# Kernel tuning notes

Measured on AMD Instinct MI355X. Metric: run time of the kernel, lower is better.

## Reference

```python
import jax, jax.numpy as jnp
import numpy as np

NUM_HEADS = 8
HEAD_DIM = 96
SCALE = HEAD_DIM ** -0.5
STRIDE_Q = (1, 2, 2)
STRIDE_KV = (1, 8, 8)
PAD = [(1, 1), (1, 1), (1, 1)]  # kernel 3 -> padding = 3//2 = 1


def _gelu_pool(t, w, stride, thw):
    """_pre_attention_pool -> GELU -> depthwise Conv3d -> _post_attention_pool.

    t: [B, H, L, hd] flattened tokens; thw = (T, Hs, Ws) with L = T*Hs*Ws.
    Returns pooled [B, H, L', hd] and new thw.
    """
    B, NH, L, C = t.shape
    T, Hs, Ws = thw
    x = t.reshape(B * NH, T, Hs, Ws, C).transpose(0, 4, 1, 2, 3)  # [B*NH, C, T, Hs, Ws]
    x = jax.nn.gelu(x, approximate=False)  # torch F.gelu default (erf)
    x = jax.lax.conv_general_dilated(
        x, w, window_strides=stride, padding=PAD,
        dimension_numbers=('NCDHW', 'OIDHW', 'NCDHW'),
        feature_group_count=C)  # depthwise: groups = head_dim
    new_thw = (x.shape[2], x.shape[3], x.shape[4])
    Lp = new_thw[0] * new_thw[1] * new_thw[2]
    x = x.reshape(B, NH, C, Lp).transpose(0, 1, 3, 2)  # [B, NH, L', C]
    return x, new_thw


def setup_inputs() -> dict:
    key = jax.random.key(0)
    ks = jax.random.split(key, 8)
    B, T, Hs, Ws, C = 2, 8, 56, 56, 768
    L = T * Hs * Ws
    s = 0.02
    return {
        'x': jax.random.normal(ks[0], (B, L, C), jnp.float32),
        'qkv_w': jax.random.normal(ks[1], (3 * C, C), jnp.float32) * s,
        'qkv_b': jnp.zeros((3 * C,), jnp.float32),
        'proj_w': jax.random.normal(ks[2], (C, C), jnp.float32) * s,
        'proj_b': jnp.zeros((C,), jnp.float32),
        'pool_q_w': jax.random.normal(ks[3], (HEAD_DIM, 1, 3, 3, 3), jnp.float32) * 0.1,
        'pool_k_w': jax.random.normal(ks[4], (HEAD_DIM, 1, 3, 3, 3), jnp.float32) * 0.1,
        'pool_v_w': jax.random.normal(ks[5], (HEAD_DIM, 1, 3, 3, 3), jnp.float32) * 0.1,
        't_size': T, 'h_size': Hs, 'w_size': Ws,
    }


def reference(x, qkv_w, qkv_b, proj_w, proj_b, pool_q_w, pool_k_w, pool_v_w,
              t_size, h_size, w_size):
    B, N, C = x.shape
    # fused qkv projection -> [3, B, heads, N, head_dim]
    qkv = (x @ qkv_w.T + qkv_b).reshape(B, N, 3, NUM_HEADS, C // NUM_HEADS)
    qkv = qkv.transpose(2, 0, 3, 1, 4)
    q, k, v = qkv[0], qkv[1], qkv[2]

    thw = (t_size, h_size, w_size)
    q, q_thw = _gelu_pool(q, pool_q_w, STRIDE_Q, thw)
    k, _ = _gelu_pool(k, pool_k_w, STRIDE_KV, thw)
    v, _ = _gelu_pool(v, pool_v_w, STRIDE_KV, thw)

    attn = jax.nn.softmax((q * SCALE) @ jnp.swapaxes(k, -2, -1), axis=-1)
    Nq = q.shape[2]
    out = (attn @ v + q)  # residual_pool=True (iMViT)
    out = out.transpose(0, 2, 1, 3).reshape(B, Nq, C)
    out = out @ proj_w.T + proj_b
    return out
```

## Files before the change

### kernel.cpp

```cpp
#include <hip/hip_runtime.h>
#include <cstdint>

#define NH 8
#define HD 96
#define CDIM 768
#define BQ 2
#define T0 8
#define H0 56
#define W0 56
#define L0 (T0*H0*W0)
#define HP_Q 28
#define WP_Q 28
#define LQ (T0*HP_Q*WP_Q)
#define HP_K 7
#define WP_K 7
#define LK (T0*HP_K*WP_K)
#define LKP 416
#define SCALE 0.10206207261596577f
#define NYC 20
#define MKV 6400

typedef __bf16 bf16;
typedef bf16 bf16x4 __attribute__((ext_vector_type(4)));
typedef bf16 bf16x8 __attribute__((ext_vector_type(8)));
typedef float f32x4 __attribute__((ext_vector_type(4)));
typedef float f4 __attribute__((ext_vector_type(4)));

#define GPTR(x) ((const __attribute__((address_space(1))) void*)(x))
#define LPTR(x) ((__attribute__((address_space(3))) void*)(x))

__device__ __forceinline__ float fast_gelu(float x) {
    float z = __builtin_fabsf(x) * 0.7071067811865476f;
    float p = 1.f + z*(0.278393f + z*(0.230389f + z*(0.000972f + z*0.078108f)));
    p = p * p;
    p = p * p;
    float e = 1.f - __builtin_amdgcn_rcpf(p);
    float erfv = (x < 0.f) ? -e : e;
    return 0.5f * x * (1.f + erfv);
}

__global__ void cvt4(const f4* __restrict__ in, bf16x4* __restrict__ out, long n4) {
    long i = (long)blockIdx.x * blockDim.x + threadIdx.x;
    long stride = (long)gridDim.x * blockDim.x;
    for (; i < n4; i += stride) {
        f4 v = in[i];
        bf16x4 o;
        o.x = (bf16)v.x; o.y = (bf16)v.y; o.z = (bf16)v.z; o.w = (bf16)v.w;
        out[i] = o;
    }
}

__device__ __forceinline__ int cmap(int i) {
    return ((i + 1) / 3) * 8 + (i + 1) % 3 - 1;
}

template<int MODE>
__global__ __launch_bounds__(256) void gemm_bt(
    const bf16* __restrict__ A, const bf16* __restrict__ B,
    const float* __restrict__ bias, void* __restrict__ Out,
    int M, int N, int K, int NBN, int gelu_cols)
{
    __shared__ bf16 sh[2*16384];
    const int tid = threadIdx.x;
    const int lane = tid & 63;
    const int w = tid >> 6;
    const int wr = w >> 1, wc = w & 1;

    const int nwg = gridDim.x;
    const int q_ = nwg >> 3, r_ = nwg & 7;
    const int xcd = blockIdx.x & 7, off = blockIdx.x >> 3;
    const int swz = (xcd < r_ ? xcd*(q_+1) : r_*(q_+1) + (xcd - r_)*q_) + off;
    const long bn = swz % NBN, bm = swz / NBN;

    f32x4 acc[4][4];
#pragma unroll
    for (int i = 0; i < 4; ++i)
#pragma unroll
        for (int j = 0; j < 4; ++j) acc[i][j] = (f32x4){0.f,0.f,0.f,0.f};

    const int trow = tid >> 3;
    const int tchunk = (tid & 7) ^ (trow & 7);

    long aoff[4];
#pragma unroll
    for (int s = 0; s < 4; ++s) {
        int rA = (int)bm*128 + s*32 + trow;
        if (MODE == 2) {
            int mm = rA < MKV ? rA : 0;
            int b = mm / 3200; int r = mm - b*3200;
            int t = r / 400;  int rr = r - t*400;
            int yi = rr / NYC, xi = rr - yi*NYC;
            int y = cmap(yi), x = cmap(xi);
            aoff[s] = ((long)b*L0 + (t*H0 + y)*W0 + x) * (long)K;
        } else {
            aoff[s] = (long)rA * K;
        }
    }
    const bf16* Bg = B + (bn*128 + trow)*(long)K + tchunk*8;

    const int arow = lane & 15;
    const int g8 = (lane >> 4) * 8;
    const int aswz = (arow & 7) * 8;

    auto stage = [&](int buf, int kt) {
        bf16* ldsA = sh + buf*16384;
        bf16* ldsB = sh + buf*16384 + 8192;
#pragma unroll
        for (int s = 0; s < 4; ++s) {
            __builtin_amdgcn_global_load_lds(GPTR(A + aoff[s] + kt*64 + tchunk*8),
                                             LPTR(ldsA + s*2048 + tid*8), 16, 0, 0);
            __builtin_amdgcn_global_load_lds(GPTR(Bg + (long)kt*64 + (long)s*32*K),
                                             LPTR(ldsB + s*2048 + tid*8), 16, 0, 0);
        }
    };
    auto compute = [&](int buf) {
        const bf16* ldsA = sh + buf*16384;
        const bf16* ldsB = sh + buf*16384 + 8192;
#pragma unroll
        for (int kk = 0; kk < 2; ++kk) {
            bf16x8 af[4], bfr[4];
#pragma unroll
            for (int i = 0; i < 4; ++i)
                af[i] = *(const bf16x8*)&ldsA[(wr*64 + i*16 + arow)*64 + ((kk*32 + g8) ^ aswz)];
#pragma unroll
            for (int j = 0; j < 4; ++j)
                bfr[j] = *(const bf16x8*)&ldsB[(wc*64 + j*16 + arow)*64 + ((kk*32 + g8) ^ aswz)];
            __builtin_amdgcn_s_setprio(1);
#pragma unroll
            for (int i = 0; i < 4; ++i)
#pragma unroll
                for (int j = 0; j < 4; ++j)
                    acc[i][j] = __builtin_amdgcn_mfma_f32_16x16x32_bf16(af[i], bfr[j], acc[i][j], 0, 0, 0);
            __builtin_amdgcn_s_setprio(0);
        }
    };

    const int nkt = K / 64;
    stage(0, 0);
    for (int kt = 0; kt < nkt; ++kt) {
        if (kt + 1 < nkt) {
            stage((kt + 1) & 1, kt + 1);
            asm volatile("s_waitcnt vmcnt(8)" ::: "memory");
        } else {
            asm volatile("s_waitcnt vmcnt(0)" ::: "memory");
        }
        __builtin_amdgcn_s_barrier();
        __builtin_amdgcn_sched_barrier(0);
        compute(kt & 1);
        __builtin_amdgcn_sched_barrier(0);
        __builtin_amdgcn_s_barrier();
    }

    if (MODE == 1) {
#pragma unroll
        for (int j = 0; j < 4; ++j) {
            const int col = (int)bn*128 + wc*64 + j*16 + (lane & 15);
            const float bcol = bias[col];
#pragma unroll
            for (int i = 0; i < 4; ++i) {
                int row0 = (int)bm*128 + wr*64 + i*16 + ((lane>>4)<<2);
#pragma unroll
                for (int r = 0; r < 4; ++r)
                    ((float*)Out)[(size_t)(row0 + r)*N + col] = acc[i][j][r] + bcol;
            }
        }
    } else {
        bf16* tls = sh;
#pragma unroll
        for (int j = 0; j < 4; ++j) {
            const int colb = (int)bn*128 + wc*64 + j*16;
            const int lcol = wc*64 + j*16 + (lane & 15);
            const float bcol = bias[colb + (lane & 15)];
            const bool do_gelu = (MODE == 2) || (colb < gelu_cols);
#pragma unroll
            for (int i = 0; i < 4; ++i) {
                int lrow0 = wr*64 + i*16 + ((lane>>4)<<2);
#pragma unroll
                for (int r = 0; r < 4; ++r) {
                    float vacc = acc[i][j][r] + bcol;
                    if (do_gelu) vacc = fast_gelu(vacc);
                    tls[(lrow0 + r)*136 + lcol] = (bf16)vacc;
                }
            }
        }
        __syncthreads();
#pragma unroll
        for (int it = 0; it < 8; ++it) {
            int idx = it*256 + tid;
            int mloc = idx >> 4;
            int ck = idx & 15;
            bf16x8 v = *(const bf16x8*)&tls[mloc*136 + ck*8];
            int m = (int)bm*128 + mloc;
            int col = (int)bn*128 + ck*8;
            if (MODE == 0) {
                int nh = col / HD;
                int c = col - nh*HD;
                int bflag = m >= L0;
                int l = m - (bflag ? L0 : 0);
                size_t addr = ((size_t)(bflag*8 + nh)*L0 + l)*HD + c;
                *(bf16x8*)&((bf16*)Out)[addr] = v;
            } else {
                if (m < MKV) {
                    int part = col / 768;
                    int cb = col - part*768;
                    int nh = cb / HD;
                    int c = cb - nh*HD;
                    int b = m / 3200; int r = m - b*3200;
                    size_t addr = ((size_t)(part*16 + b*8 + nh)*3200 + r)*HD + c;
                    *(bf16x8*)&((bf16*)Out)[addr] = v;
                }
            }
        }
    }
}

__global__ __launch_bounds__(256) void dwconv_q(
    const bf16* __restrict__ in, const float* __restrict__ w,
    bf16* __restrict__ out, int total)
{
    __shared__ float lw[27*HD];
    for (int i = threadIdx.x; i < 27*HD; i += 256) {
        int c = i / 27, tap = i % 27;
        lw[tap*HD + c] = w[i];
    }
    __syncthreads();
    int idx = blockIdx.x*256 + threadIdx.x;
    if (idx >= total) return;
    int c8 = idx % 12;
    int p = idx / 12;
    int xo = p % WP_Q;
    int yo = (p / WP_Q) % HP_Q;
    int bh = p / (WP_Q*HP_Q);
    const bf16* ip = in + (size_t)bh * L0 * HD + c8*8;

    float acc[T0][8];
#pragma unroll
    for (int t = 0; t < T0; ++t)
#pragma unroll
        for (int j = 0; j < 8; ++j) acc[t][j] = 0.f;

#pragma unroll
    for (int dy = 0; dy < 3; ++dy) {
        int y = yo*2 + dy - 1;
        if ((unsigned)y >= (unsigned)H0) continue;
#pragma unroll
        for (int dx = 0; dx < 3; ++dx) {
            int x = xo*2 + dx - 1;
            if ((unsigned)x >= (unsigned)W0) continue;
            float wreg[3][8];
#pragma unroll
            for (int dt = 0; dt < 3; ++dt)
#pragma unroll
                for (int j = 0; j < 8; ++j)
                    wreg[dt][j] = lw[(dt*9 + dy*3 + dx)*HD + c8*8 + j];
            const bf16* colp = ip + ((size_t)(y*W0 + x))*HD;
#pragma unroll
            for (int t = 0; t < T0; ++t) {
                bf16x8 v = *(const bf16x8*)(colp + (size_t)t*H0*W0*HD);
                float f[8];
#pragma unroll
                for (int j = 0; j < 8; ++j) f[j] = (float)v[j];
#pragma unroll
                for (int dt = 0; dt < 3; ++dt) {
                    int to = t - dt + 1;
                    if (to < 0 || to >= T0) continue;
#pragma unroll
                    for (int j = 0; j < 8; ++j)
                        acc[to][j] += wreg[dt][j] * f[j];
                }
            }
        }
    }

#pragma unroll
    for (int to = 0; to < T0; ++to) {
        int l = (to*HP_Q + yo)*WP_Q + xo;
        bf16x8 ov;
#pragma unroll
        for (int j = 0; j < 8; ++j) ov[j] = (bf16)acc[to][j];
        *(bf16x8*)&out[((size_t)bh*LQ + l)*HD + c8*8] = ov;
    }
}

template<int MODE>
__global__ __launch_bounds__(256) void dwconv_kv(
    const bf16* __restrict__ in, const float* __restrict__ w,
    bf16* __restrict__ out, int total)
{
    __shared__ float lw[27*HD];
    for (int i = threadIdx.x; i < 27*HD; i += 256) {
        int c = i / 27, tap = i % 27;
        lw[tap*HD + c] = w[i];
    }
    __syncthreads();
    int idx = blockIdx.x*256 + threadIdx.x;
    if (idx >= total) return;
    int c8 = idx % 12;
    int p = idx / 12;
    int xo = p % WP_K;
    int yo = (p / WP_K) % HP_K;
    int bh = p / (WP_K*HP_K);
    const bf16* ip = in + (size_t)bh * 3200 * HD + c8*8;

    float acc[T0][8];
#pragma unroll
    for (int t = 0; t < T0; ++t)
#pragma unroll
        for (int j = 0; j < 8; ++j) acc[t][j] = 0.f;

#pragma unroll
    for (int dy = 0; dy < 3; ++dy) {
        int yi = 3*yo + dy - 1;
        if ((unsigned)yi >= (unsigned)NYC) continue;
#pragma unroll
        for (int dx = 0; dx < 3; ++dx) {
            int xi = 3*xo + dx - 1;
            if ((unsigned)xi >= (unsigned)NYC) continue;
            float wreg[3][8];
#pragma unroll
            for (int dt = 0; dt < 3; ++dt)
#pragma unroll
                for (int j = 0; j < 8; ++j)
                    wreg[dt][j] = lw[(dt*9 + dy*3 + dx)*HD + c8*8 + j];
            const bf16* colp = ip + ((size_t)(yi*NYC + xi))*HD;
#pragma unroll
            for (int t = 0; t < T0; ++t) {
                bf16x8 v = *(const bf16x8*)(colp + (size_t)t*400*HD);
                float f[8];
#pragma unroll
                for (int j = 0; j < 8; ++j) f[j] = (float)v[j];
#pragma unroll
                for (int dt = 0; dt < 3; ++dt) {
                    int to = t - dt + 1;
                    if (to < 0 || to >= T0) continue;
#pragma unroll
                    for (int j = 0; j < 8; ++j)
                        acc[to][j] += wreg[dt][j] * f[j];
                }
            }
        }
    }

#pragma unroll
    for (int to = 0; to < T0; ++to) {
        int l = (to*HP_K + yo)*WP_K + xo;
        if (MODE == 2) {
#pragma unroll
            for (int j = 0; j < 8; ++j)
                out[((size_t)bh*HD + c8*8 + j)*LKP + l] = (bf16)acc[to][j];
        } else {
            bf16x8 ov;
#pragma unroll
            for (int j = 0; j < 8; ++j) ov[j] = (bf16)acc[to][j];
            *(bf16x8*)&out[((size_t)bh*LKP + l)*HD + c8*8] = ov;
        }
    }
}

__global__ __launch_bounds__(256) void attn_mfma(
    const bf16* __restrict__ q, const bf16* __restrict__ k,
    const bf16* __restrict__ vt, bf16* __restrict__ out)
{
    const int tid = threadIdx.x;
    const int lane = tid & 63;
    const int w = tid >> 6;
    const int col = lane & 15;
    const int g = lane >> 4;
    const int blk = blockIdx.x;
    const int qblk = blk % (LQ/64);
    const int bh = blk / (LQ/64);
    const int q0 = qblk*64 + w*16;

    const bf16* Qp  = q  + ((size_t)bh*LQ + q0)*HD;
    const bf16* Kp  = k  + (size_t)bh*LKP*HD;
    const bf16* VTp = vt + (size_t)bh*HD*LKP;

    bf16x8 qf[3];
#pragma unroll
    for (int c = 0; c < 3; ++c)
        qf[c] = *(const bf16x8*)&Qp[(size_t)col*HD + c*32 + g*8];

    f32x4 o[6];
#pragma unroll
    for (int t = 0; t < 6; ++t) o[t] = (f32x4){0.f,0.f,0.f,0.f};
    float lsum = 0.f;

    for (int kc = 0; kc < LKP/32; ++kc) {
        const int kvb = kc*32;
        uint32_t P[2][2];
#pragma unroll
        for (int s = 0; s < 2; ++s) {
            f32x4 acc = (f32x4){0.f,0.f,0.f,0.f};
#pragma unroll
            for (int c = 0; c < 3; ++c) {
                bf16x8 kf = *(const bf16x8*)&Kp[(size_t)(kvb + s*16 + col)*HD + c*32 + g*8];
                acc = __builtin_amdgcn_mfma_f32_16x16x32_bf16(kf, qf[c], acc, 0, 0, 0);
            }
            bf16x4 pb;
#pragma unroll
            for (int r = 0; r < 4; ++r) {
                int kv = kvb + s*16 + g*4 + r;
                float p = (kv < LK) ? __expf(acc[r]*SCALE) : 0.f;
                lsum += p;
                pb[r] = (bf16)p;
            }
            union { bf16x4 v; uint32_t u[2]; } pk; pk.v = pb;
            P[s][0] = pk.u[0]; P[s][1] = pk.u[1];
        }
        uint32_t sa0 = (g < 2) ? P[1][0] : P[0][0];
        uint32_t sa1 = (g < 2) ? P[1][1] : P[0][1];
        uint32_t tb0 = (g < 2) ? P[0][0] : P[1][0];
        uint32_t tb1 = (g < 2) ? P[0][1] : P[1][1];
        uint32_t R32_0 = (uint32_t)__shfl_xor((int)sa0, 32);
        uint32_t R32_1 = (uint32_t)__shfl_xor((int)sa1, 32);
        uint32_t R48_0 = (uint32_t)__shfl_xor((int)sa0, 48);
        uint32_t R48_1 = (uint32_t)__shfl_xor((int)sa1, 48);
        uint32_t R16_0 = (uint32_t)__shfl_xor((int)tb0, 16);
        uint32_t R16_1 = (uint32_t)__shfl_xor((int)tb1, 16);
        union { uint32_t u[4]; bf16x8 v; } pf;
        pf.u[0] = (g == 0) ? P[0][0] : (g == 1) ? R48_0 : (g == 2) ? R32_0 : R16_0;
        pf.u[1] = (g == 0) ? P[0][1] : (g == 1) ? R48_1 : (g == 2) ? R32_1 : R16_1;
        pf.u[2] = (g == 0) ? R16_0 : (g == 1) ? R32_0 : (g == 2) ? R48_0 : P[1][0];
        pf.u[3] = (g == 0) ? R16_1 : (g == 1) ? R32_1 : (g == 2) ? R48_1 : P[1][1];
#pragma unroll
        for (int t = 0; t < 6; ++t) {
            bf16x8 vf = *(const bf16x8*)&VTp[(size_t)(t*16 + col)*LKP + kvb + g*8];
            o[t] = __builtin_amdgcn_mfma_f32_16x16x32_bf16(vf, pf.v, o[t], 0, 0, 0);
        }
    }

    lsum += __shfl_xor(lsum, 16);
    lsum += __shfl_xor(lsum, 32);
    float inv = 1.f / lsum;

    const int b = bh >> 3, nh = bh & 7;
    size_t obase = ((size_t)b*LQ + q0 + col)*CDIM + (size_t)nh*HD;
#pragma unroll
    for (int t = 0; t < 6; ++t) {
        bf16x4 qres = *(const bf16x4*)&Qp[(size_t)col*HD + t*16 + g*4];
        bf16x4 ov;
#pragma unroll
        for (int r = 0; r < 4; ++r)
            ov[r] = (bf16)(o[t][r]*inv + (float)qres[r]);
        *(bf16x4*)&out[obase + t*16 + g*4] = ov;
    }
}

extern "C" void kernel_launch(void* const* d_in, const int* in_sizes, int n_in,
                              void* d_out, int out_size, void* d_ws, size_t ws_size,
                              hipStream_t stream) {
    const float* x      = (const float*)d_in[0];
    const float* qkv_w  = (const float*)d_in[1];
    const float* qkv_b  = (const float*)d_in[2];
    const float* proj_w = (const float*)d_in[3];
    const float* proj_b = (const float*)d_in[4];
    const float* pq_w   = (const float*)d_in[5];
    const float* pk_w   = (const float*)d_in[6];
    const float* pv_w   = (const float*)d_in[7];

    uint8_t* ws = (uint8_t*)d_ws;
    bf16* x_bf     = (bf16*)(ws);
    bf16* qg_out   = (bf16*)(ws +  77070336);
    bf16* kv_c     = (bf16*)(ws + 154140672);
    bf16* wqkv_bf  = (bf16*)(ws + 173801472);
    bf16* wproj_bf = (bf16*)(ws + 177340416);
    bf16* q_bf     = (bf16*)(ws + 178520064);
    bf16* k_bf     = (bf16*)(ws + 197787648);
    bf16* vt_bf    = (bf16*)(ws + 199065600);
    bf16* attn_o   = (bf16*)(ws + 200343552);

    hipMemsetAsync(k_bf, 0, 1277952, stream);
    hipMemsetAsync(vt_bf, 0, 1277952, stream);

    cvt4<<<2048, 256, 0, stream>>>((const f4*)x, (bf16x4*)x_bf, 38535168/4);
    cvt4<<<1728, 256, 0, stream>>>((const f4*)qkv_w, (bf16x4*)wqkv_bf, 1769472/4);
    cvt4<<<576, 256, 0, stream>>>((const f4*)proj_w, (bf16x4*)wproj_bf, 589824/4);

    gemm_bt<0><<<392*6, 256, 0, stream>>>(
        x_bf, wqkv_bf, qkv_b, qg_out, 50176, 768, 768, 6, 768);

    gemm_bt<2><<<50*12, 256, 0, stream>>>(
        x_bf, wqkv_bf + (size_t)768*768, qkv_b + 768, kv_c, MKV, 1536, 768, 12, 0);

    dwconv_q<<<588, 256, 0, stream>>>(qg_out, pq_w, q_bf, 16*HP_Q*WP_Q*12);
    dwconv_kv<1><<<37, 256, 0, stream>>>(kv_c, pk_w, k_bf, 16*HP_K*WP_K*12);
    dwconv_kv<2><<<37, 256, 0, stream>>>(kv_c + (size_t)16*3200*HD, pv_w, vt_bf, 16*HP_K*WP_K*12);

    attn_mfma<<<16*(LQ/64), 256, 0, stream>>>(q_bf, k_bf, vt_bf, attn_o);

    gemm_bt<1><<<6*98, 256, 0, stream>>>(
        attn_o, wproj_bf, proj_b, d_out, 12544, 768, 768, 6, 0);
}
```

Baseline: 340.9 us.

## Use 256x256-tile GEMM for Q projection and fuse conversion and KV conv launches

Replaces the 128x128 Q-projection GEMM with a dedicated 512-thread 256x256-tile kernel. It uses direct global-to-LDS loads interleaved with MFMA phases, double buffering, and a GELU epilogue. It also merges the three fp32->bf16 conversions into one launch, and merges the K and V depthwise convs into one launch that zeroes the padding, removing two memsets. The intent is more data reuse in the largest GEMM and less launch overhead, at the cost of higher register/LDS pressure. The MODE 2 row clamp is removed, which may read past MKV rows for the last tile.

```diff
diff --git a/kernel.cpp b/kernel.cpp
--- a/kernel.cpp
+++ b/kernel.cpp
@@ -39,26 +39,164 @@
     return 0.5f * x * (1.f + erfv);
 }
 
-__global__ void cvt4(const f4* __restrict__ in, bf16x4* __restrict__ out, long n4) {
-    long i = (long)blockIdx.x * blockDim.x + threadIdx.x;
+#define NX4 9633792
+#define NW4 442368
+#define NP4 147456
+__global__ void cvt_all(const f4* __restrict__ x, const f4* __restrict__ wq,
+                        const f4* __restrict__ wp, bf16x4* __restrict__ xo,
+                        bf16x4* __restrict__ wqo, bf16x4* __restrict__ wpo) {
+    const long total = (long)NX4 + NW4 + NP4;
     long stride = (long)gridDim.x * blockDim.x;
-    for (; i < n4; i += stride) {
-        f4 v = in[i];
-        bf16x4 o;
-        o.x = (bf16)v.x; o.y = (bf16)v.y; o.z = (bf16)v.z; o.w = (bf16)v.w;
-        out[i] = o;
+    for (long i = (long)blockIdx.x * blockDim.x + threadIdx.x; i < total; i += stride) {
+        f4 v; bf16x4* o;
+        if (i < NX4)            { v = x[i];            o = xo + i; }
+        else if (i < NX4 + NW4) { v = wq[i - NX4];     o = wqo + (i - NX4); }
+        else                    { v = wp[i - NX4 - NW4]; o = wpo + (i - NX4 - NW4); }
+        bf16x4 t;
+        t.x = (bf16)v.x; t.y = (bf16)v.y; t.z = (bf16)v.z; t.w = (bf16)v.w;
+        *o = t;
     }
 }
 
 __device__ __forceinline__ int cmap(int i) {
     return ((i + 1) / 3) * 8 + (i + 1) % 3 - 1;
+}
+
+__global__ __launch_bounds__(512, 2) void gemm256_q(
+    const bf16* __restrict__ A, const bf16* __restrict__ B,
+    const float* __restrict__ bias, bf16* __restrict__ Out)
+{
+    __shared__ bf16 sh[2*32768];
+    const int tid = threadIdx.x;
+    const int lane = tid & 63;
+    const int wid = tid >> 6;
+    const int wm = wid >> 2, wn = wid & 3;
+    const int arow = lane & 15;
+    const int g = lane >> 4;
+    const int srow = tid >> 3;
+    const int schunk = tid & 7;
+    const int csw = schunk ^ (srow & 7);
+    const int K = 768;
+
+    const int nwg = gridDim.x;
+    const int q_ = nwg >> 3, r_ = nwg & 7;
+    const int xcd = blockIdx.x & 7, off = blockIdx.x >> 3;
+    const int swz = (xcd < r_ ? xcd*(q_+1) : r_*(q_+1) + (xcd - r_)*q_) + off;
+    const long bn = swz % 3, bm = swz / 3;
+
+    f32x4 acc[8][4];
+#pragma unroll
+    for (int i = 0; i < 8; ++i)
+#pragma unroll
+        for (int j = 0; j < 4; ++j) acc[i][j] = (f32x4){0.f,0.f,0.f,0.f};
+
+    const bf16* Ab = A + (bm*256 + srow)*(long)K + csw*8;
+    const bf16* Bb = B + (bn*256 + srow)*(long)K + csw*8;
+
+    auto issueA = [&](int buf, int kt, int s) {
+        __builtin_amdgcn_global_load_lds(GPTR(Ab + (long)(s*64)*K + kt*64),
+            LPTR(sh + buf*32768 + s*4096 + tid*8), 16, 0, 0);
+    };
+    auto issueB = [&](int buf, int kt, int s) {
+        __builtin_amdgcn_global_load_lds(GPTR(Bb + (long)(s*64)*K + kt*64),
+            LPTR(sh + buf*32768 + 16384 + s*4096 + tid*8), 16, 0, 0);
+    };
+    auto phase = [&](int buf, int qm, int qn) {
+        const bf16* ldsA = sh + buf*32768;
+        const bf16* ldsB = sh + buf*32768 + 16384;
+        bf16x8 af[4][2], bfr[2][2];
+#pragma unroll
+        for (int i = 0; i < 4; ++i) {
+            int R = wm*128 + (qm*4 + i)*16 + arow;
+#pragma unroll
+            for (int kk = 0; kk < 2; ++kk)
+                af[i][kk] = *(const bf16x8*)&ldsA[R*64 + (((kk*4 + g) ^ (R & 7))*8)];
+        }
+#pragma unroll
+        for (int j = 0; j < 2; ++j) {
+            int R = wn*64 + (qn*2 + j)*16 + arow;
+#pragma unroll
+            for (int kk = 0; kk < 2; ++kk)
+                bfr[j][kk] = *(const bf16x8*)&ldsB[R*64 + (((kk*4 + g) ^ (R & 7))*8)];
+        }
+        asm volatile("s_waitcnt lgkmcnt(0)" ::: "memory");
+        __builtin_amdgcn_sched_barrier(0);
+        __builtin_amdgcn_s_setprio(1);
+#pragma unroll
+        for (int i = 0; i < 4; ++i)
+#pragma unroll
+            for (int j = 0; j < 2; ++j)
+#pragma unroll
+                for (int kk = 0; kk < 2; ++kk)
+                    acc[qm*4 + i][qn*2 + j] = __builtin_amdgcn_mfma_f32_16x16x32_bf16(
+                        af[i][kk], bfr[j][kk], acc[qm*4 + i][qn*2 + j], 0, 0, 0);
+        __builtin_amdgcn_s_setprio(0);
+        __builtin_amdgcn_sched_barrier(0);
+    };
+
+    const int nkt = K / 64;
+#pragma unroll
+    for (int s = 0; s < 4; ++s) { issueA(0, 0, s); issueB(0, 0, s); }
+
+    for (int kt = 0; kt < nkt; ++kt) {
+        const int cur = kt & 1, nxt = cur ^ 1;
+        const bool pre = (kt + 1 < nkt);
+        if (pre) { issueA(nxt, kt+1, 0); issueA(nxt, kt+1, 1); }
+        if (pre) asm volatile("s_waitcnt vmcnt(2)" ::: "memory");
+        else     asm volatile("s_waitcnt vmcnt(0)" ::: "memory");
+        __builtin_amdgcn_s_barrier();
+        phase(cur, 0, 0);
+        if (pre) { issueA(nxt, kt+1, 2); issueA(nxt, kt+1, 3); }
+        phase(cur, 0, 1);
+        if (pre) { issueB(nxt, kt+1, 0); issueB(nxt, kt+1, 1); }
+        phase(cur, 1, 0);
+        if (pre) { issueB(nxt, kt+1, 2); issueB(nxt, kt+1, 3); }
+        phase(cur, 1, 1);
+        __builtin_amdgcn_s_barrier();
+    }
+
+    bf16* tls = sh;
+#pragma unroll 1
+    for (int half = 0; half < 2; ++half) {
+        __syncthreads();
+        if (wm == half) {
+#pragma unroll
+            for (int mf = 0; mf < 8; ++mf) {
+                int rowl = mf*16 + (g << 2);
+#pragma unroll
+                for (int nf = 0; nf < 4; ++nf) {
+                    int coll = wn*64 + nf*16 + arow;
+                    float bcol = bias[bn*256 + coll];
+#pragma unroll
+                    for (int r = 0; r < 4; ++r)
+                        tls[(rowl + r)*264 + coll] = (bf16)fast_gelu(acc[mf][nf][r] + bcol);
+                }
+            }
+        }
+        __syncthreads();
+#pragma unroll
+        for (int it = 0; it < 8; ++it) {
+            int idx = it*512 + tid;
+            int mloc = idx >> 5;
+            int ck = idx & 31;
+            bf16x8 v = *(const bf16x8*)&tls[mloc*264 + ck*8];
+            int m = (int)bm*256 + half*128 + mloc;
+            int col = (int)bn*256 + ck*8;
+            int nh = col / HD;
+            int c = col - nh*HD;
+            int bflag = m >= L0;
+            int l = m - (bflag ? L0 : 0);
+            size_t addr = ((size_t)(bflag*8 + nh)*L0 + l)*HD + c;
+            *(bf16x8*)&Out[addr] = v;
+        }
+    }
 }
 
 template<int MODE>
 __global__ __launch_bounds__(256) void gemm_bt(
     const bf16* __restrict__ A, const bf16* __restrict__ B,
     const float* __restrict__ bias, void* __restrict__ Out,
-    int M, int N, int K, int NBN, int gelu_cols)
+    int M, int N, int K, int NBN)
 {
     __shared__ bf16 sh[2*16384];
     const int tid = threadIdx.x;
@@ -86,8 +224,7 @@
     for (int s = 0; s < 4; ++s) {
         int rA = (int)bm*128 + s*32 + trow;
         if (MODE == 2) {
-            int mm = rA < MKV ? rA : 0;
-            int b = mm / 3200; int r = mm - b*3200;
+            int b = rA / 3200; int r = rA - b*3200;
             int t = r / 400;  int rr = r - t*400;
             int yi = rr / NYC, xi = rr - yi*NYC;
             int y = cmap(yi), x = cmap(xi);
@@ -171,16 +308,12 @@
             const int colb = (int)bn*128 + wc*64 + j*16;
             const int lcol = wc*64 + j*16 + (lane & 15);
             const float bcol = bias[colb + (lane & 15)];
-            const bool do_gelu = (MODE == 2) || (colb < gelu_cols);
 #pragma unroll
             for (int i = 0; i < 4; ++i) {
                 int lrow0 = wr*64 + i*16 + ((lane>>4)<<2);
 #pragma unroll
-                for (int r = 0; r < 4; ++r) {
-                    float vacc = acc[i][j][r] + bcol;
-                    if (do_gelu) vacc = fast_gelu(vacc);
-                    tls[(lrow0 + r)*136 + lcol] = (bf16)vacc;
-                }
+                for (int r = 0; r < 4; ++r)
+                    tls[(lrow0 + r)*136 + lcol] = (bf16)fast_gelu(acc[i][j][r] + bcol);
             }
         }
         __syncthreads();
@@ -192,24 +325,13 @@
             bf16x8 v = *(const bf16x8*)&tls[mloc*136 + ck*8];
             int m = (int)bm*128 + mloc;
             int col = (int)bn*128 + ck*8;
-            if (MODE == 0) {
-                int nh = col / HD;
-                int c = col - nh*HD;
-                int bflag = m >= L0;
-                int l = m - (bflag ? L0 : 0);
-                size_t addr = ((size_t)(bflag*8 + nh)*L0 + l)*HD + c;
-                *(bf16x8*)&((bf16*)Out)[addr] = v;
-            } else {
-                if (m < MKV) {
-                    int part = col / 768;
-                    int cb = col - part*768;
-                    int nh = cb / HD;
-                    int c = cb - nh*HD;
-                    int b = m / 3200; int r = m - b*3200;
-                    size_t addr = ((size_t)(part*16 + b*8 + nh)*3200 + r)*HD + c;
-                    *(bf16x8*)&((bf16*)Out)[addr] = v;
-                }
-            }
+            int part = col / 768;
+            int cb = col - part*768;
+            int nh = cb / HD;
+            int c = cb - nh*HD;
+            int b = m / 3200; int r = m - b*3200;
+            size_t addr = ((size_t)(part*16 + b*8 + nh)*3200 + r)*HD + c;
+            *(bf16x8*)&((bf16*)Out)[addr] = v;
         }
     }
 }
@@ -282,19 +404,41 @@
     }
 }
 
-template<int MODE>
-__global__ __launch_bounds__(256) void dwconv_kv(
-    const bf16* __restrict__ in, const float* __restrict__ w,
-    bf16* __restrict__ out, int total)
+__global__ __launch_bounds__(256) void dwconv_kv_all(
+    const bf16* __restrict__ kv, const float* __restrict__ wk,
+    const float* __restrict__ wv, bf16* __restrict__ kout, bf16* __restrict__ vtout)
 {
+    const int seg = blockIdx.x / 40;
+    const int lb  = blockIdx.x % 40;
+    const float* w = seg ? wv : wk;
+    const bf16* in = kv + (size_t)seg * 16 * 3200 * HD;
     __shared__ float lw[27*HD];
     for (int i = threadIdx.x; i < 27*HD; i += 256) {
         int c = i / 27, tap = i % 27;
         lw[tap*HD + c] = w[i];
     }
     __syncthreads();
-    int idx = blockIdx.x*256 + threadIdx.x;
-    if (idx >= total) return;
+
+    if (lb >= 37) {
+        int pid = (lb - 37)*256 + threadIdx.x;
+        if (seg == 0) {
+            for (int e = pid; e < 16*24*96; e += 768) {
+                int bh = e / (24*96); int rem = e - bh*24*96;
+                int l = LK + rem / 96; int c = rem % 96;
+                kout[((size_t)bh*LKP + l)*HD + c] = (bf16)0.f;
+            }
+        } else {
+            for (int e = pid; e < 16*96*24; e += 768) {
+                int bh = e / (96*24); int rem = e - bh*96*24;
+                int c = rem / 24; int l = LK + rem % 24;
+                vtout[((size_t)bh*HD + c)*LKP + l] = (bf16)0.f;
+            }
+        }
+        return;
+    }
+
+    int idx = lb*256 + threadIdx.x;
+    if (idx >= 16*HP_K*WP_K*12) return;
     int c8 = idx % 12;
     int p = idx / 12;
     int xo = p % WP_K;
@@ -344,15 +488,15 @@
 #pragma unroll
     for (int to = 0; to < T0; ++to) {
         int l = (to*HP_K + yo)*WP_K + xo;
-        if (MODE == 2) {
+        if (seg == 1) {
 #pragma unroll
             for (int j = 0; j < 8; ++j)
-                out[((size_t)bh*HD + c8*8 + j)*LKP + l] = (bf16)acc[to][j];
+                vtout[((size_t)bh*HD + c8*8 + j)*LKP + l] = (bf16)acc[to][j];
         } else {
             bf16x8 ov;
 #pragma unroll
             for (int j = 0; j < 8; ++j) ov[j] = (bf16)acc[to][j];
-            *(bf16x8*)&out[((size_t)bh*LKP + l)*HD + c8*8] = ov;
+            *(bf16x8*)&kout[((size_t)bh*LKP + l)*HD + c8*8] = ov;
         }
     }
 }
@@ -469,25 +613,19 @@
     bf16* vt_bf    = (bf16*)(ws + 199065600);
     bf16* attn_o   = (bf16*)(ws + 200343552);
 
-    hipMemsetAsync(k_bf, 0, 1277952, stream);
-    hipMemsetAsync(vt_bf, 0, 1277952, stream);
-
-    cvt4<<<2048, 256, 0, stream>>>((const f4*)x, (bf16x4*)x_bf, 38535168/4);
-    cvt4<<<1728, 256, 0, stream>>>((const f4*)qkv_w, (bf16x4*)wqkv_bf, 1769472/4);
-    cvt4<<<576, 256, 0, stream>>>((const f4*)proj_w, (bf16x4*)wproj_bf, 589824/4);
-
-    gemm_bt<0><<<392*6, 256, 0, stream>>>(
-        x_bf, wqkv_bf, qkv_b, qg_out, 50176, 768, 768, 6, 768);
+    cvt_all<<<2560, 256, 0, stream>>>((const f4*)x, (const f4*)qkv_w, (const f4*)proj_w,
+                                      (bf16x4*)x_bf, (bf16x4*)wqkv_bf, (bf16x4*)wproj_bf);
+
+    gemm256_q<<<196*3, 512, 0, stream>>>(x_bf, wqkv_bf, qkv_b, qg_out);
 
     gemm_bt<2><<<50*12, 256, 0, stream>>>(
-        x_bf, wqkv_bf + (size_t)768*768, qkv_b + 768, kv_c, MKV, 1536, 768, 12, 0);
+        x_bf, wqkv_bf + (size_t)768*768, qkv_b + 768, kv_c, MKV, 1536, 768, 12);
 
     dwconv_q<<<588, 256, 0, stream>>>(qg_out, pq_w, q_bf, 16*HP_Q*WP_Q*12);
-    dwconv_kv<1><<<37, 256, 0, stream>>>(kv_c, pk_w, k_bf, 16*HP_K*WP_K*12);
-    dwconv_kv<2><<<37, 256, 0, stream>>>(kv_c + (size_t)16*3200*HD, pv_w, vt_bf, 16*HP_K*WP_K*12);
+    dwconv_kv_all<<<80, 256, 0, stream>>>(kv_c, pk_w, pv_w, k_bf, vt_bf);
 
     attn_mfma<<<16*(LQ/64), 256, 0, stream>>>(q_bf, k_bf, vt_bf, attn_o);
 
     gemm_bt<1><<<6*98, 256, 0, stream>>>(
-        attn_o, wproj_bf, proj_b, d_out, 12544, 768, 768, 6, 0);
-}
+        attn_o, wproj_bf, proj_b, d_out, 12544, 768, 768, 6);
+}
```

Measured after the change: 326.3 us. -4.3%, faster.
